# Kernel optimization log

Hardware: AMD Instinct MI355X
Metric: run time of the kernel (lower is better)

## Reference

```python
import jax, jax.numpy as jnp
import numpy as np

N_EMBD = 1024
N_HEAD = 16
BLOCK_SIZE = 2048


def setup_inputs() -> dict:
    key = jax.random.key(0)
    k1, k2, k3 = jax.random.split(key, 3)
    B, T, C = 2, 2048, N_EMBD
    x = jax.random.normal(k1, (B, T, C), dtype=jnp.float32)
    # Dense(3*n_embd, use_bias=False): kernel [C, 3C]
    Wqkv = jax.random.normal(k2, (C, 3 * C), dtype=jnp.float32) * (1.0 / np.sqrt(C))
    # Output Dense(n_embd): kernel [C, C] + bias [C]
    Wout = jax.random.normal(k3, (C, C), dtype=jnp.float32) * (1.0 / np.sqrt(C))
    bout = jnp.zeros((C,), dtype=jnp.float32)
    return {"x": x, "Wqkv": Wqkv, "Wout": Wout, "bout": bout}


def reference(x, Wqkv, Wout, bout):
    B, T, C = x.shape
    H = N_HEAD
    hs = C // H  # head_size

    qkv = x @ Wqkv                       # [B, T, 3C]
    q, k, v = jnp.split(qkv, 3, axis=-1)  # each [B, T, C]
    q = q.reshape(B, T, H, hs).transpose(0, 2, 1, 3)  # [B, H, T, hs]
    k = k.reshape(B, T, H, hs).transpose(0, 2, 1, 3)
    v = v.reshape(B, T, H, hs).transpose(0, 2, 1, 3)

    att = jnp.einsum("bhqd,bhkd->bhqk", q, k) * (hs ** -0.5)  # [B, H, T, T]
    T_use = min(T, BLOCK_SIZE)
    mask = jnp.tril(jnp.ones((T_use, T_use), dtype=bool))
    att = jnp.where(mask, att, -jnp.inf)
    att = jax.nn.softmax(att, axis=-1)
    # dropout: deterministic (training=False) -> identity

    out = jnp.einsum("bhqk,bhkd->bhqd", att, v)  # [B, H, T, hs]
    out = out.transpose(0, 2, 1, 3).reshape(B, T, C)
    out = out @ Wout + bout
    return out
```

## Files before the change

### kernel.cpp

```cpp
#include <hip/hip_runtime.h>
#include <cstdint>
#include <cstddef>

#define BB 2
#define TT 2048
#define CC 1024
#define HH 16
#define HS 64
#define MM (BB*TT)
#define N1 (3*CC)

#define PST2 40

#define QSCALE 0.1803368801111243f

typedef __bf16 bf16_t;
typedef bf16_t bf16x8 __attribute__((ext_vector_type(8)));
typedef float  floatx4 __attribute__((ext_vector_type(4)));

__device__ __forceinline__ bf16_t f2bf(float f) {
    uint32_t u = __builtin_bit_cast(uint32_t, f);
    u += 0x7FFFu + ((u >> 16) & 1u);
    unsigned short s = (unsigned short)(u >> 16);
    return __builtin_bit_cast(bf16_t, s);
}

__device__ __forceinline__ void load_lds16(const bf16_t* g, bf16_t* l) {
    __builtin_amdgcn_global_load_lds((__attribute__((address_space(1))) void*)g,
                                     (__attribute__((address_space(3))) void*)l,
                                     16, 0, 0);
}

__global__ __launch_bounds__(256) void k_pack(const float* __restrict__ src,
                                              bf16_t* __restrict__ dst) {
    size_t i = ((size_t)blockIdx.x * 256 + threadIdx.x) * 8;
    float4 a = *(const float4*)(src + i);
    float4 b = *(const float4*)(src + i + 4);
    bf16x8 o;
    o[0] = f2bf(a.x); o[1] = f2bf(a.y); o[2] = f2bf(a.z); o[3] = f2bf(a.w);
    o[4] = f2bf(b.x); o[5] = f2bf(b.y); o[6] = f2bf(b.z); o[7] = f2bf(b.w);
    *(bf16x8*)(dst + i) = o;
}

__global__ __launch_bounds__(256) void k_transpose(const float* __restrict__ src,
                                                   bf16_t* __restrict__ dst,
                                                   int R, int Ccol) {
    __shared__ bf16_t tile[32][33];
    int c0 = blockIdx.x * 32, r0 = blockIdx.y * 32;
    int tx = threadIdx.x, ty = threadIdx.y;
    for (int i = ty; i < 32; i += 8)
        tile[i][tx] = f2bf(src[(size_t)(r0 + i) * Ccol + c0 + tx]);
    __syncthreads();
    for (int i = ty; i < 32; i += 8)
        dst[(size_t)(c0 + i) * R + r0 + tx] = tile[tx][i];
}

__device__ __forceinline__ void gemm_core(const bf16_t* __restrict__ A,
                                          const bf16_t* __restrict__ Bt,
                                          bf16_t* As, bf16_t* Bs,
                                          int m0, int n0, int K,
                                          floatx4 acc[4][4]) {
    const int tid = threadIdx.x;
    const int wave = tid >> 6, lane = tid & 63;
    const int quad = lane >> 4, lrow = lane & 15;
    const int wm = wave >> 1, wn = wave & 1;
    const int lsub = lane >> 2;
    const int kc = lane & 3;

    for (int kk = 0; kk < K; kk += 32) {
        for (int s = 0; s < 2; ++s) {
            int rg = wave * 2 + s;
            const bf16_t* ga = A  + (size_t)(m0 + rg * 16 + lsub) * K + kk + kc * 8;
            const bf16_t* gb = Bt + (size_t)(n0 + rg * 16 + lsub) * K + kk + kc * 8;
            load_lds16(ga, As + rg * 512);
            load_lds16(gb, Bs + rg * 512);
        }
        __syncthreads();
        bf16x8 af[4], bfr[4];
        for (int i = 0; i < 4; ++i)
            af[i] = *(const bf16x8*)(As + (wm * 64 + i * 16 + lrow) * 32 + quad * 8);
        for (int j = 0; j < 4; ++j)
            bfr[j] = *(const bf16x8*)(Bs + (wn * 64 + j * 16 + lrow) * 32 + quad * 8);
        for (int i = 0; i < 4; ++i)
            for (int j = 0; j < 4; ++j)
                acc[i][j] = __builtin_amdgcn_mfma_f32_16x16x32_bf16(af[i], bfr[j], acc[i][j], 0, 0, 0);
        __syncthreads();
    }
}

__global__ __launch_bounds__(256, 2) void k_gemm_qkv(const bf16_t* __restrict__ x,
                                                     const bf16_t* __restrict__ Wt,
                                                     bf16_t* __restrict__ qb,
                                                     bf16_t* __restrict__ kb,
                                                     bf16_t* __restrict__ vn) {
    __shared__ bf16_t As[128 * 32];
    __shared__ bf16_t Bs[128 * 32];
    const int m0 = blockIdx.y * 128, n0 = blockIdx.x * 128;
    floatx4 acc[4][4];
    for (int i = 0; i < 4; ++i)
        for (int j = 0; j < 4; ++j)
            acc[i][j] = floatx4{0.f, 0.f, 0.f, 0.f};
    gemm_core(x, Wt, As, Bs, m0, n0, CC, acc);

    const int tid = threadIdx.x, wave = tid >> 6, lane = tid & 63;
    const int quad = lane >> 4, lrow = lane & 15;
    const int wm = wave >> 1, wn = wave & 1;
    for (int i = 0; i < 4; ++i)
        for (int j = 0; j < 4; ++j) {
            int gn = n0 + wn * 64 + j * 16 + lrow;
            int which = gn >> 10, c = gn & 1023, h = c >> 6, d = c & 63;
            for (int r = 0; r < 4; ++r) {
                int gm = m0 + wm * 64 + i * 16 + quad * 4 + r;
                int b = gm >> 11, t = gm & 2047;
                float val = acc[i][j][r];
                if (which == 0)
                    qb[((size_t)(b * HH + h) * TT + t) * HS + d] = f2bf(val * QSCALE);
                else if (which == 1)
                    kb[((size_t)(b * HH + h) * TT + t) * HS + d] = f2bf(val);
                else
                    vn[((size_t)(b * HH + h) * TT + t) * HS + d] = f2bf(val);
            }
        }
}

__global__ __launch_bounds__(256) void k_vperm(const bf16_t* __restrict__ vn,
                                               bf16_t* __restrict__ vt) {
    __shared__ bf16_t tile[64][72];
    const int tid = threadIdx.x;
    const int bh = blockIdx.x & 31, tb = blockIdx.x >> 5;
    const bf16_t* src = vn + ((size_t)bh * TT + tb * 64) * HS;

    for (int h = 0; h < 2; ++h) {
        int r = (tid >> 3) + h * 32;
        int c8 = (tid & 7) * 8;
        *(bf16x8*)(&tile[r][c8]) = *(const bf16x8*)(src + (size_t)r * HS + c8);
    }
    __syncthreads();

    bf16_t* dst = vt + (size_t)bh * HS * TT + tb * 64;
    const int a   = tid & 15;
    const int blk = ((tid >> 4) & 1) * 32;
    const int dg  = tid >> 5;
    for (int k = 0; k < 8; ++k) {
        int d = dg * 8 + k;
        uint32_t lo = (uint32_t)__builtin_bit_cast(unsigned short, tile[blk + a][d]);
        uint32_t hi = (uint32_t)__builtin_bit_cast(unsigned short, tile[blk + a + 16][d]);
        *(uint32_t*)(dst + (size_t)d * TT + blk + 2 * a) = lo | (hi << 16);
    }
}

__device__ static const signed char ORD[48][2] = {
    {15,-1},{31,0},{31,1},{30,0},{30,1},
    {14,-1},{29,0},{29,1},{28,0},{28,1},
    {13,-1},{27,0},{27,1},{26,0},{26,1},
    {12,-1},{25,0},{25,1},{24,0},{24,1},
    {11,-1},{23,0},{23,1},{22,0},{22,1},
    {10,-1},{21,0},{21,1},{20,0},{20,1},
    { 9,-1},{19,0},{19,1},{18,0},{18,1},
    { 8,-1},{17,0},{17,1},{16,0},{16,1},
    { 7,-1},{ 6,-1},{ 5,-1},{ 4,-1},{ 3,-1},{ 2,-1},{ 1,-1},{ 0,-1}
};

__global__ __launch_bounds__(128, 2) void k_attn(const bf16_t* __restrict__ qb,
                                                 const bf16_t* __restrict__ kb,
                                                 const bf16_t* __restrict__ vt,
                                                 float* __restrict__ o0,
                                                 float* __restrict__ o1,
                                                 float* __restrict__ l0,
                                                 float* __restrict__ l1) {
    __shared__ bf16_t Kb[2][32 * 72];
    __shared__ bf16_t Vb[2][64 * 40];
    __shared__ bf16_t Ps[2][2][32 * PST2];
    const int tid = threadIdx.x;
    const int w = tid >> 6, lane = tid & 63;
    const int quad = lane >> 4, lrow = lane & 15;
    const int bh = blockIdx.x & 31;
    const int j = blockIdx.x >> 5;
    const int qg = ORD[j][0];
    const int cc = ORD[j][1];
    const int ct = (cc < 0) ? (2 * qg + 2) : (qg + 1);
    const int key0 = (cc == 1) ? (qg + 1) * 32 : 0;
    const int kendl = 2 * qg + w + 1 - ((cc == 1) ? (qg + 1) : 0);
    const int kw = min(kendl, ct);
    const int q0 = qg * 64 + w * 32;

    const bf16_t* Qg = qb + (size_t)bh * TT * HS;
    const bf16_t* Kg = kb + (size_t)bh * TT * HS;
    const bf16_t* Vg = vt + (size_t)bh * HS * TT;

    const int skey = tid >> 2, scol = (tid & 3) * 16;
    const int svrow = tid >> 1, svcol = (tid & 1) * 16;

    bf16x8 kra, krb, vra, vrb;
    {
        const bf16_t* gk = Kg + (size_t)(key0 + skey) * HS + scol;
        kra = *(const bf16x8*)(gk);
        krb = *(const bf16x8*)(gk + 8);
        const bf16_t* gv = Vg + (size_t)svrow * TT + key0 + svcol;
        vra = *(const bf16x8*)(gv);
        vrb = *(const bf16x8*)(gv + 8);
        *(bf16x8*)(&Kb[0][skey * 72 + scol])     = kra;
        *(bf16x8*)(&Kb[0][skey * 72 + scol + 8]) = krb;
        *(bf16x8*)(&Vb[0][svrow * 40 + svcol])     = vra;
        *(bf16x8*)(&Vb[0][svrow * 40 + svcol + 8]) = vrb;
    }

    bf16x8 aq[2][2];
    for (int tq = 0; tq < 2; ++tq)
        for (int c = 0; c < 2; ++c)
            aq[tq][c] = *(const bf16x8*)(Qg + (size_t)(q0 + tq * 16 + lrow) * HS + c * 32 + quad * 8);

    const bf16_t onebf = __builtin_bit_cast(bf16_t, (unsigned short)0x3F80);
    bf16x8 bones = {onebf, onebf, onebf, onebf, onebf, onebf, onebf, onebf};

    floatx4 o[2][4];
    for (int tq = 0; tq < 2; ++tq)
        for (int dc = 0; dc < 4; ++dc) o[tq][dc] = floatx4{0.f, 0.f, 0.f, 0.f};
    floatx4 ol[2] = {floatx4{0.f,0.f,0.f,0.f}, floatx4{0.f,0.f,0.f,0.f}};

    bf16x8 bv_sav[4];
    const int wrow0 = quad * 4;

    for (int t = 0; t < ct; ++t) {
        __syncthreads();
        if (t + 1 < ct) {
            const bf16_t* gk = Kg + (size_t)(key0 + (t + 1) * 32 + skey) * HS + scol;
            kra = *(const bf16x8*)(gk);
            krb = *(const bf16x8*)(gk + 8);
            const bf16_t* gv = Vg + (size_t)svrow * TT + key0 + (t + 1) * 32 + svcol;
            vra = *(const bf16x8*)(gv);
            vrb = *(const bf16x8*)(gv + 8);
        }
        if (t < kw) {
            if (t > 0) {
                const bf16_t* Pp = &Ps[w][(t - 1) & 1][0];
                bf16x8 pa0 = *(const bf16x8*)(Pp + (size_t)lrow * PST2 + quad * 8);
                bf16x8 pa1 = *(const bf16x8*)(Pp + (size_t)(16 + lrow) * PST2 + quad * 8);
                o[0][0] = __builtin_amdgcn_mfma_f32_16x16x32_bf16(pa0, bv_sav[0], o[0][0], 0, 0, 0);
                o[0][1] = __builtin_amdgcn_mfma_f32_16x16x32_bf16(pa0, bv_sav[1], o[0][1], 0, 0, 0);
                o[0][2] = __builtin_amdgcn_mfma_f32_16x16x32_bf16(pa0, bv_sav[2], o[0][2], 0, 0, 0);
                o[0][3] = __builtin_amdgcn_mfma_f32_16x16x32_bf16(pa0, bv_sav[3], o[0][3], 0, 0, 0);
                ol[0]   = __builtin_amdgcn_mfma_f32_16x16x32_bf16(pa0, bones, ol[0], 0, 0, 0);
                o[1][0] = __builtin_amdgcn_mfma_f32_16x16x32_bf16(pa1, bv_sav[0], o[1][0], 0, 0, 0);
                o[1][1] = __builtin_amdgcn_mfma_f32_16x16x32_bf16(pa1, bv_sav[1], o[1][1], 0, 0, 0);
                o[1][2] = __builtin_amdgcn_mfma_f32_16x16x32_bf16(pa1, bv_sav[2], o[1][2], 0, 0, 0);
                o[1][3] = __builtin_amdgcn_mfma_f32_16x16x32_bf16(pa1, bv_sav[3], o[1][3], 0, 0, 0);
                ol[1]   = __builtin_amdgcn_mfma_f32_16x16x32_bf16(pa1, bones, ol[1], 0, 0, 0);
            }
            const bf16_t* Kt = &Kb[t & 1][0];
            const bf16_t* Vt = &Vb[t & 1][0];
            bf16x8 bk0 = *(const bf16x8*)(Kt + lrow * 72 + quad * 8);
            bf16x8 bk1 = *(const bf16x8*)(Kt + lrow * 72 + 32 + quad * 8);
            bf16x8 bk2 = *(const bf16x8*)(Kt + (16 + lrow) * 72 + quad * 8);
            bf16x8 bk3 = *(const bf16x8*)(Kt + (16 + lrow) * 72 + 32 + quad * 8);
            floatx4 s00 = floatx4{0.f,0.f,0.f,0.f}, s01 = s00, s10 = s00, s11 = s00;
            s00 = __builtin_amdgcn_mfma_f32_16x16x32_bf16(aq[0][0], bk0, s00, 0, 0, 0);
            s00 = __builtin_amdgcn_mfma_f32_16x16x32_bf16(aq[0][1], bk1, s00, 0, 0, 0);
            s01 = __builtin_amdgcn_mfma_f32_16x16x32_bf16(aq[0][0], bk2, s01, 0, 0, 0);
            s01 = __builtin_amdgcn_mfma_f32_16x16x32_bf16(aq[0][1], bk3, s01, 0, 0, 0);
            s10 = __builtin_amdgcn_mfma_f32_16x16x32_bf16(aq[1][0], bk0, s10, 0, 0, 0);
            s10 = __builtin_amdgcn_mfma_f32_16x16x32_bf16(aq[1][1], bk1, s10, 0, 0, 0);
            s11 = __builtin_amdgcn_mfma_f32_16x16x32_bf16(aq[1][0], bk2, s11, 0, 0, 0);
            s11 = __builtin_amdgcn_mfma_f32_16x16x32_bf16(aq[1][1], bk3, s11, 0, 0, 0);

            bv_sav[0] = *(const bf16x8*)(Vt + (0  + lrow) * 40 + quad * 8);
            bv_sav[1] = *(const bf16x8*)(Vt + (16 + lrow) * 40 + quad * 8);
            bv_sav[2] = *(const bf16x8*)(Vt + (32 + lrow) * 40 + quad * 8);
            bv_sav[3] = *(const bf16x8*)(Vt + (48 + lrow) * 40 + quad * 8);

            uint32_t* P32 = (uint32_t*)(&Ps[w][t & 1][0]);
            if (t < kendl - 1) {
                for (int r = 0; r < 4; ++r) {
                    float e00 = __builtin_amdgcn_exp2f(s00[r]);
                    float e01 = __builtin_amdgcn_exp2f(s01[r]);
                    float e10 = __builtin_amdgcn_exp2f(s10[r]);
                    float e11 = __builtin_amdgcn_exp2f(s11[r]);
                    uint32_t pk0 = __builtin_amdgcn_perm(
                        __builtin_bit_cast(uint32_t, e01),
                        __builtin_bit_cast(uint32_t, e00), 0x07060302u);
                    uint32_t pk1 = __builtin_amdgcn_perm(
                        __builtin_bit_cast(uint32_t, e11),
                        __builtin_bit_cast(uint32_t, e10), 0x07060302u);
                    P32[(wrow0 + r) * 20 + lrow]      = pk0;
                    P32[(wrow0 + r + 16) * 20 + lrow] = pk1;
                }
            } else {
                for (int r = 0; r < 4; ++r) {
                    bool keep = lrow <= quad * 4 + r;
                    float e00 = keep ? __builtin_amdgcn_exp2f(s00[r]) : 0.f;
                    float e01 = 0.f; (void)s01;
                    float e10 = __builtin_amdgcn_exp2f(s10[r]);
                    float e11 = keep ? __builtin_amdgcn_exp2f(s11[r]) : 0.f;
                    uint32_t pk0 = __builtin_amdgcn_perm(
                        __builtin_bit_cast(uint32_t, e01),
                        __builtin_bit_cast(uint32_t, e00), 0x07060302u);
                    uint32_t pk1 = __builtin_amdgcn_perm(
                        __builtin_bit_cast(uint32_t, e11),
                        __builtin_bit_cast(uint32_t, e10), 0x07060302u);
                    P32[(wrow0 + r) * 20 + lrow]      = pk0;
                    P32[(wrow0 + r + 16) * 20 + lrow] = pk1;
                }
            }
        }
        if (t + 1 < ct) {
            bf16_t* Kn = &Kb[(t + 1) & 1][0];
            bf16_t* Vn = &Vb[(t + 1) & 1][0];
            *(bf16x8*)(Kn + skey * 72 + scol)     = kra;
            *(bf16x8*)(Kn + skey * 72 + scol + 8) = krb;
            *(bf16x8*)(Vn + svrow * 40 + svcol)     = vra;
            *(bf16x8*)(Vn + svrow * 40 + svcol + 8) = vrb;
        }
    }

    asm volatile("s_waitcnt lgkmcnt(0)" ::: "memory");
    {
        const bf16_t* Pp = &Ps[w][(kw - 1) & 1][0];
        bf16x8 pa0 = *(const bf16x8*)(Pp + (size_t)lrow * PST2 + quad * 8);
        bf16x8 pa1 = *(const bf16x8*)(Pp + (size_t)(16 + lrow) * PST2 + quad * 8);
        o[0][0] = __builtin_amdgcn_mfma_f32_16x16x32_bf16(pa0, bv_sav[0], o[0][0], 0, 0, 0);
        o[0][1] = __builtin_amdgcn_mfma_f32_16x16x32_bf16(pa0, bv_sav[1], o[0][1], 0, 0, 0);
        o[0][2] = __builtin_amdgcn_mfma_f32_16x16x32_bf16(pa0, bv_sav[2], o[0][2], 0, 0, 0);
        o[0][3] = __builtin_amdgcn_mfma_f32_16x16x32_bf16(pa0, bv_sav[3], o[0][3], 0, 0, 0);
        ol[0]   = __builtin_amdgcn_mfma_f32_16x16x32_bf16(pa0, bones, ol[0], 0, 0, 0);
        o[1][0] = __builtin_amdgcn_mfma_f32_16x16x32_bf16(pa1, bv_sav[0], o[1][0], 0, 0, 0);
        o[1][1] = __builtin_amdgcn_mfma_f32_16x16x32_bf16(pa1, bv_sav[1], o[1][1], 0, 0, 0);
        o[1][2] = __builtin_amdgcn_mfma_f32_16x16x32_bf16(pa1, bv_sav[2], o[1][2], 0, 0, 0);
        o[1][3] = __builtin_amdgcn_mfma_f32_16x16x32_bf16(pa1, bv_sav[3], o[1][3], 0, 0, 0);
        ol[1]   = __builtin_amdgcn_mfma_f32_16x16x32_bf16(pa1, bones, ol[1], 0, 0, 0);
    }

    for (int tq = 0; tq < 2; ++tq)
        for (int r = 0; r < 4; ++r) {
            int q = q0 + tq * 16 + quad * 4 + r;
            if (cc == 1) {
                float* dst = o1 + ((size_t)(bh * 16 + qg - 16) * 64 + (q - qg * 64)) * 64 + lrow;
                for (int dc = 0; dc < 4; ++dc) dst[dc * 16] = o[tq][dc][r];
                if (lrow == 0) l1[(size_t)(bh * 16 + qg - 16) * 64 + (q - qg * 64)] = ol[tq][r];
            } else {
                float* dst = o0 + ((size_t)bh * TT + q) * HS + lrow;
                for (int dc = 0; dc < 4; ++dc) dst[dc * 16] = o[tq][dc][r];
                if (lrow == 0) l0[(size_t)bh * TT + q] = ol[tq][r];
            }
        }
}

__global__ __launch_bounds__(256) void k_norm(const float* __restrict__ o0,
                                              const float* __restrict__ o1,
                                              const float* __restrict__ l0,
                                              const float* __restrict__ l1,
                                              bf16_t* __restrict__ yb) {
    int idx = blockIdx.x * 256 + threadIdx.x;
    int d8 = idx & 7;
    int q  = (idx >> 3) & (TT - 1);
    int bh = idx >> 14;
    const float* s0 = o0 + ((size_t)bh * TT + q) * HS + d8 * 8;
    float4 a = *(const float4*)(s0);
    float4 b = *(const float4*)(s0 + 4);
    float l = l0[(size_t)bh * TT + q];
    int qg = q >> 6;
    if (qg >= 16) {
        const float* s1 = o1 + ((size_t)(bh * 16 + qg - 16) * 64 + (q & 63)) * 64 + d8 * 8;
        float4 a1 = *(const float4*)(s1);
        float4 b1 = *(const float4*)(s1 + 4);
        a.x += a1.x; a.y += a1.y; a.z += a1.z; a.w += a1.w;
        b.x += b1.x; b.y += b1.y; b.z += b1.z; b.w += b1.w;
        l += l1[(size_t)(bh * 16 + qg - 16) * 64 + (q & 63)];
    }
    float inv = 1.0f / l;
    bf16x8 r;
    r[0] = f2bf(a.x * inv); r[1] = f2bf(a.y * inv);
    r[2] = f2bf(a.z * inv); r[3] = f2bf(a.w * inv);
    r[4] = f2bf(b.x * inv); r[5] = f2bf(b.y * inv);
    r[6] = f2bf(b.z * inv); r[7] = f2bf(b.w * inv);
    int bb = bh >> 4, h = bh & 15;
    *(bf16x8*)(yb + ((size_t)(bb * TT + q)) * CC + h * HS + d8 * 8) = r;
}

__global__ __launch_bounds__(256, 2) void k_gemm_out(const bf16_t* __restrict__ yin,
                                                     const bf16_t* __restrict__ Wt,
                                                     const float* __restrict__ bias,
                                                     float* __restrict__ out) {
    __shared__ bf16_t As[128 * 32];
    __shared__ bf16_t Bs[128 * 32];
    const int m0 = blockIdx.y * 128, n0 = blockIdx.x * 128;
    floatx4 acc[4][4];
    for (int i = 0; i < 4; ++i)
        for (int j = 0; j < 4; ++j)
            acc[i][j] = floatx4{0.f, 0.f, 0.f, 0.f};
    gemm_core(yin, Wt, As, Bs, m0, n0, CC, acc);

    const int tid = threadIdx.x, wave = tid >> 6, lane = tid & 63;
    const int quad = lane >> 4, lrow = lane & 15;
    const int wm = wave >> 1, wn = wave & 1;
    for (int i = 0; i < 4; ++i)
        for (int j = 0; j < 4; ++j) {
            int gn = n0 + wn * 64 + j * 16 + lrow;
            float bb = bias[gn];
            for (int r = 0; r < 4; ++r) {
                int gm = m0 + wm * 64 + i * 16 + quad * 4 + r;
                out[(size_t)gm * CC + gn] = acc[i][j][r] + bb;
            }
        }
}

extern "C" void kernel_launch(void* const* d_in, const int* in_sizes, int n_in,
                              void* d_out, int out_size, void* d_ws, size_t ws_size,
                              hipStream_t stream) {
    (void)in_sizes; (void)n_in; (void)out_size; (void)ws_size;
    const float* x    = (const float*)d_in[0];
    const float* Wqkv = (const float*)d_in[1];
    const float* Wout = (const float*)d_in[2];
    const float* bout = (const float*)d_in[3];
    float* out = (float*)d_out;

    bf16_t* xb  = (bf16_t*)d_ws;
    bf16_t* Wt1 = xb + (size_t)MM * CC;
    bf16_t* Wt2 = Wt1 + (size_t)N1 * CC;
    bf16_t* qb  = Wt2 + (size_t)CC * CC;
    bf16_t* kb  = qb + (size_t)BB * HH * TT * HS;
    bf16_t* vb  = kb + (size_t)BB * HH * TT * HS;
    bf16_t* yb  = vb + (size_t)BB * HH * TT * HS;
    bf16_t* vn  = yb;
    float*  o0  = (float*)d_out;
    float*  o1  = (float*)xb;
    float*  l0  = (float*)Wt1;
    float*  l1  = l0 + (size_t)BB * HH * TT;

    k_pack<<<dim3((size_t)MM * CC / (256 * 8)), 256, 0, stream>>>(x, xb);
    k_transpose<<<dim3(N1 / 32, CC / 32), dim3(32, 8), 0, stream>>>(Wqkv, Wt1, CC, N1);
    k_transpose<<<dim3(CC / 32, CC / 32), dim3(32, 8), 0, stream>>>(Wout, Wt2, CC, CC);
    k_gemm_qkv<<<dim3(N1 / 128, MM / 128), 256, 0, stream>>>(xb, Wt1, qb, kb, vn);
    k_vperm<<<dim3(32 * 32), 256, 0, stream>>>(vn, vb);
    k_attn<<<dim3(48 * 32), 128, 0, stream>>>(qb, kb, vb, o0, o1, l0, l1);
    k_norm<<<dim3(BB * HH * TT * 8 / 256), 256, 0, stream>>>(o0, o1, l0, l1, yb);
    k_gemm_out<<<dim3(CC / 128, MM / 128), 256, 0, stream>>>(yb, Wt2, bout, out);
}
```

Measured before the change: 190.4 us.

## Fuse prep kernels, write V transposed from QKV GEMM, normalize unsplit rows in attention

Merges the x pack and both weight transposes into one launch. The QKV GEMM epilogue now writes V directly in transposed layout with packed 16-byte stores, so the separate V permute kernel is gone. Attention blocks that hold a whole row (cc<0) normalize and write bf16 output themselves. k_norm then only merges the split halves for the upper 1024 queries. This removes several launches and intermediate fp32 round trips, but the epilogue and attention tail become more complex.

```diff
diff --git a/kernel.cpp b/kernel.cpp
--- a/kernel.cpp
+++ b/kernel.cpp
@@ -31,28 +31,41 @@
                                      16, 0, 0);
 }
 
-__global__ __launch_bounds__(256) void k_pack(const float* __restrict__ src,
-                                              bf16_t* __restrict__ dst) {
-    size_t i = ((size_t)blockIdx.x * 256 + threadIdx.x) * 8;
-    float4 a = *(const float4*)(src + i);
-    float4 b = *(const float4*)(src + i + 4);
-    bf16x8 o;
-    o[0] = f2bf(a.x); o[1] = f2bf(a.y); o[2] = f2bf(a.z); o[3] = f2bf(a.w);
-    o[4] = f2bf(b.x); o[5] = f2bf(b.y); o[6] = f2bf(b.z); o[7] = f2bf(b.w);
-    *(bf16x8*)(dst + i) = o;
-}
-
-__global__ __launch_bounds__(256) void k_transpose(const float* __restrict__ src,
-                                                   bf16_t* __restrict__ dst,
-                                                   int R, int Ccol) {
-    __shared__ bf16_t tile[32][33];
-    int c0 = blockIdx.x * 32, r0 = blockIdx.y * 32;
-    int tx = threadIdx.x, ty = threadIdx.y;
+__device__ __forceinline__ void transpose_body(const float* __restrict__ src,
+                                               bf16_t* __restrict__ dst,
+                                               int R, int Ccol, int bx, int by,
+                                               int tx, int ty, bf16_t (*tile)[33]) {
+    int c0 = bx * 32, r0 = by * 32;
     for (int i = ty; i < 32; i += 8)
         tile[i][tx] = f2bf(src[(size_t)(r0 + i) * Ccol + c0 + tx]);
     __syncthreads();
     for (int i = ty; i < 32; i += 8)
         dst[(size_t)(c0 + i) * R + r0 + tx] = tile[tx][i];
+}
+
+__global__ __launch_bounds__(256) void k_prep(const float* __restrict__ x,
+                                              const float* __restrict__ Wqkv,
+                                              const float* __restrict__ Wout,
+                                              bf16_t* __restrict__ xb,
+                                              bf16_t* __restrict__ Wt1,
+                                              bf16_t* __restrict__ Wt2) {
+    __shared__ bf16_t tile[32][33];
+    const int bid = blockIdx.x, tid = threadIdx.x;
+    if (bid < 2048) {
+        size_t i = ((size_t)bid * 256 + tid) * 8;
+        float4 a = *(const float4*)(x + i);
+        float4 b = *(const float4*)(x + i + 4);
+        bf16x8 o;
+        o[0] = f2bf(a.x); o[1] = f2bf(a.y); o[2] = f2bf(a.z); o[3] = f2bf(a.w);
+        o[4] = f2bf(b.x); o[5] = f2bf(b.y); o[6] = f2bf(b.z); o[7] = f2bf(b.w);
+        *(bf16x8*)(xb + i) = o;
+    } else if (bid < 2048 + 3072) {
+        int bb = bid - 2048;
+        transpose_body(Wqkv, Wt1, CC, N1, bb % 96, bb / 96, tid & 31, tid >> 5, tile);
+    } else {
+        int bb = bid - 5120;
+        transpose_body(Wout, Wt2, CC, CC, bb & 31, bb >> 5, tid & 31, tid >> 5, tile);
+    }
 }
 
 __device__ __forceinline__ void gemm_core(const bf16_t* __restrict__ A,
@@ -92,7 +105,7 @@
                                                      const bf16_t* __restrict__ Wt,
                                                      bf16_t* __restrict__ qb,
                                                      bf16_t* __restrict__ kb,
-                                                     bf16_t* __restrict__ vn) {
+                                                     bf16_t* __restrict__ vt) {
     __shared__ bf16_t As[128 * 32];
     __shared__ bf16_t Bs[128 * 32];
     const int m0 = blockIdx.y * 128, n0 = blockIdx.x * 128;
@@ -105,47 +118,33 @@
     const int tid = threadIdx.x, wave = tid >> 6, lane = tid & 63;
     const int quad = lane >> 4, lrow = lane & 15;
     const int wm = wave >> 1, wn = wave & 1;
-    for (int i = 0; i < 4; ++i)
-        for (int j = 0; j < 4; ++j) {
-            int gn = n0 + wn * 64 + j * 16 + lrow;
-            int which = gn >> 10, c = gn & 1023, h = c >> 6, d = c & 63;
-            for (int r = 0; r < 4; ++r) {
-                int gm = m0 + wm * 64 + i * 16 + quad * 4 + r;
-                int b = gm >> 11, t = gm & 2047;
-                float val = acc[i][j][r];
-                if (which == 0)
-                    qb[((size_t)(b * HH + h) * TT + t) * HS + d] = f2bf(val * QSCALE);
-                else if (which == 1)
-                    kb[((size_t)(b * HH + h) * TT + t) * HS + d] = f2bf(val);
-                else
-                    vn[((size_t)(b * HH + h) * TT + t) * HS + d] = f2bf(val);
-            }
-        }
-}
-
-__global__ __launch_bounds__(256) void k_vperm(const bf16_t* __restrict__ vn,
-                                               bf16_t* __restrict__ vt) {
-    __shared__ bf16_t tile[64][72];
-    const int tid = threadIdx.x;
-    const int bh = blockIdx.x & 31, tb = blockIdx.x >> 5;
-    const bf16_t* src = vn + ((size_t)bh * TT + tb * 64) * HS;
-
-    for (int h = 0; h < 2; ++h) {
-        int r = (tid >> 3) + h * 32;
-        int c8 = (tid & 7) * 8;
-        *(bf16x8*)(&tile[r][c8]) = *(const bf16x8*)(src + (size_t)r * HS + c8);
-    }
-    __syncthreads();
-
-    bf16_t* dst = vt + (size_t)bh * HS * TT + tb * 64;
-    const int a   = tid & 15;
-    const int blk = ((tid >> 4) & 1) * 32;
-    const int dg  = tid >> 5;
-    for (int k = 0; k < 8; ++k) {
-        int d = dg * 8 + k;
-        uint32_t lo = (uint32_t)__builtin_bit_cast(unsigned short, tile[blk + a][d]);
-        uint32_t hi = (uint32_t)__builtin_bit_cast(unsigned short, tile[blk + a + 16][d]);
-        *(uint32_t*)(dst + (size_t)d * TT + blk + 2 * a) = lo | (hi << 16);
+    const int b = m0 >> 11;
+    for (int j = 0; j < 4; ++j) {
+        int gn = n0 + wn * 64 + j * 16 + lrow;
+        int which = gn >> 10, c = gn & 1023, h = c >> 6, d = c & 63;
+        if (which == 0) {
+            for (int i = 0; i < 4; ++i)
+                for (int r = 0; r < 4; ++r) {
+                    int t = (m0 & 2047) + wm * 64 + i * 16 + quad * 4 + r;
+                    qb[((size_t)(b * HH + h) * TT + t) * HS + d] = f2bf(acc[i][j][r] * QSCALE);
+                }
+        } else if (which == 1) {
+            for (int i = 0; i < 4; ++i)
+                for (int r = 0; r < 4; ++r) {
+                    int t = (m0 & 2047) + wm * 64 + i * 16 + quad * 4 + r;
+                    kb[((size_t)(b * HH + h) * TT + t) * HS + d] = f2bf(acc[i][j][r]);
+                }
+        } else {
+            for (int a = 0; a < 2; ++a) {
+                bf16x8 pv;
+                for (int r = 0; r < 4; ++r) {
+                    pv[r * 2]     = f2bf(acc[2 * a][j][r]);
+                    pv[r * 2 + 1] = f2bf(acc[2 * a + 1][j][r]);
+                }
+                int tb2 = (m0 & 2047) + wm * 64 + a * 32;
+                *(bf16x8*)(vt + ((size_t)(b * HH + h) * HS + d) * TT + tb2 + quad * 8) = pv;
+            }
+        }
     }
 }
 
@@ -164,6 +163,7 @@
 __global__ __launch_bounds__(128, 2) void k_attn(const bf16_t* __restrict__ qb,
                                                  const bf16_t* __restrict__ kb,
                                                  const bf16_t* __restrict__ vt,
+                                                 bf16_t* __restrict__ yb,
                                                  float* __restrict__ o0,
                                                  float* __restrict__ o1,
                                                  float* __restrict__ l0,
@@ -329,19 +329,33 @@
         ol[1]   = __builtin_amdgcn_mfma_f32_16x16x32_bf16(pa1, bones, ol[1], 0, 0, 0);
     }
 
-    for (int tq = 0; tq < 2; ++tq)
-        for (int r = 0; r < 4; ++r) {
-            int q = q0 + tq * 16 + quad * 4 + r;
-            if (cc == 1) {
+    if (cc < 0) {
+        const int b = bh >> 4, h = bh & 15;
+        for (int tq = 0; tq < 2; ++tq)
+            for (int r = 0; r < 4; ++r) {
+                float inv = 1.0f / ol[tq][r];
+                int q = q0 + tq * 16 + quad * 4 + r;
+                for (int dc = 0; dc < 4; ++dc)
+                    yb[(size_t)(b * TT + q) * CC + h * HS + dc * 16 + lrow] =
+                        f2bf(o[tq][dc][r] * inv);
+            }
+    } else if (cc == 1) {
+        for (int tq = 0; tq < 2; ++tq)
+            for (int r = 0; r < 4; ++r) {
+                int q = q0 + tq * 16 + quad * 4 + r;
                 float* dst = o1 + ((size_t)(bh * 16 + qg - 16) * 64 + (q - qg * 64)) * 64 + lrow;
                 for (int dc = 0; dc < 4; ++dc) dst[dc * 16] = o[tq][dc][r];
                 if (lrow == 0) l1[(size_t)(bh * 16 + qg - 16) * 64 + (q - qg * 64)] = ol[tq][r];
-            } else {
+            }
+    } else {
+        for (int tq = 0; tq < 2; ++tq)
+            for (int r = 0; r < 4; ++r) {
+                int q = q0 + tq * 16 + quad * 4 + r;
                 float* dst = o0 + ((size_t)bh * TT + q) * HS + lrow;
                 for (int dc = 0; dc < 4; ++dc) dst[dc * 16] = o[tq][dc][r];
                 if (lrow == 0) l0[(size_t)bh * TT + q] = ol[tq][r];
             }
-        }
+    }
 }
 
 __global__ __launch_bounds__(256) void k_norm(const float* __restrict__ o0,
@@ -351,21 +365,18 @@
                                               bf16_t* __restrict__ yb) {
     int idx = blockIdx.x * 256 + threadIdx.x;
     int d8 = idx & 7;
-    int q  = (idx >> 3) & (TT - 1);
-    int bh = idx >> 14;
+    int q  = 1024 + ((idx >> 3) & 1023);
+    int bh = idx >> 13;
+    int qg = q >> 6;
     const float* s0 = o0 + ((size_t)bh * TT + q) * HS + d8 * 8;
+    const float* s1 = o1 + ((size_t)(bh * 16 + qg - 16) * 64 + (q & 63)) * 64 + d8 * 8;
     float4 a = *(const float4*)(s0);
     float4 b = *(const float4*)(s0 + 4);
-    float l = l0[(size_t)bh * TT + q];
-    int qg = q >> 6;
-    if (qg >= 16) {
-        const float* s1 = o1 + ((size_t)(bh * 16 + qg - 16) * 64 + (q & 63)) * 64 + d8 * 8;
-        float4 a1 = *(const float4*)(s1);
-        float4 b1 = *(const float4*)(s1 + 4);
-        a.x += a1.x; a.y += a1.y; a.z += a1.z; a.w += a1.w;
-        b.x += b1.x; b.y += b1.y; b.z += b1.z; b.w += b1.w;
-        l += l1[(size_t)(bh * 16 + qg - 16) * 64 + (q & 63)];
-    }
+    float4 a1 = *(const float4*)(s1);
+    float4 b1 = *(const float4*)(s1 + 4);
+    a.x += a1.x; a.y += a1.y; a.z += a1.z; a.w += a1.w;
+    b.x += b1.x; b.y += b1.y; b.z += b1.z; b.w += b1.w;
+    float l = l0[(size_t)bh * TT + q] + l1[(size_t)(bh * 16 + qg - 16) * 64 + (q & 63)];
     float inv = 1.0f / l;
     bf16x8 r;
     r[0] = f2bf(a.x * inv); r[1] = f2bf(a.y * inv);
@@ -420,18 +431,14 @@
     bf16_t* kb  = qb + (size_t)BB * HH * TT * HS;
     bf16_t* vb  = kb + (size_t)BB * HH * TT * HS;
     bf16_t* yb  = vb + (size_t)BB * HH * TT * HS;
-    bf16_t* vn  = yb;
     float*  o0  = (float*)d_out;
     float*  o1  = (float*)xb;
     float*  l0  = (float*)Wt1;
     float*  l1  = l0 + (size_t)BB * HH * TT;
 
-    k_pack<<<dim3((size_t)MM * CC / (256 * 8)), 256, 0, stream>>>(x, xb);
-    k_transpose<<<dim3(N1 / 32, CC / 32), dim3(32, 8), 0, stream>>>(Wqkv, Wt1, CC, N1);
-    k_transpose<<<dim3(CC / 32, CC / 32), dim3(32, 8), 0, stream>>>(Wout, Wt2, CC, CC);
-    k_gemm_qkv<<<dim3(N1 / 128, MM / 128), 256, 0, stream>>>(xb, Wt1, qb, kb, vn);
-    k_vperm<<<dim3(32 * 32), 256, 0, stream>>>(vn, vb);
-    k_attn<<<dim3(48 * 32), 128, 0, stream>>>(qb, kb, vb, o0, o1, l0, l1);
-    k_norm<<<dim3(BB * HH * TT * 8 / 256), 256, 0, stream>>>(o0, o1, l0, l1, yb);
+    k_prep<<<dim3(2048 + 3072 + 1024), 256, 0, stream>>>(x, Wqkv, Wout, xb, Wt1, Wt2);
+    k_gemm_qkv<<<dim3(N1 / 128, MM / 128), 256, 0, stream>>>(xb, Wt1, qb, kb, vb);
+    k_attn<<<dim3(48 * 32), 128, 0, stream>>>(qb, kb, vb, yb, o0, o1, l0, l1);
+    k_norm<<<dim3(1024), 256, 0, stream>>>(o0, o1, l0, l1, yb);
     k_gemm_out<<<dim3(CC / 128, MM / 128), 256, 0, stream>>>(yb, Wt2, bout, out);
 }
```

Result: faster. 179.3 us (-5.8%).
